# Kernel tuning notes

Hardware: AMD Instinct MI355X
Metric: run time of the kernel (lower is better)

The kernel has to match this reference:

```python
import jax, jax.numpy as jnp
import numpy as np

DIM = 768
NUM_HEADS = 12
POLY_DEG = 3
GRID = (24, 24)
BATCH = 16


def _make_powers():
    H, W = GRID
    ii, jj = np.meshgrid(np.arange(H), np.arange(W), indexing='ij')
    coords = np.stack([ii.ravel(), jj.ravel()], axis=-1).astype(np.float32)  # [HW, 2]
    dists = np.abs(coords[:, None, :] - coords[None, :, :]).sum(-1)  # L1 cdist [HW, HW]
    powers = np.stack([dists ** i for i in range(POLY_DEG + 1)], axis=0)  # [deg+1, HW, HW]
    return jnp.asarray(powers, dtype=jnp.float32)


def setup_inputs() -> dict:
    key = jax.random.key(0)
    ks = jax.random.split(key, 5)
    N = GRID[0] * GRID[1] + 1  # 577
    x = jax.random.normal(ks[0], (BATCH, N, DIM), dtype=jnp.float32)
    # nn.Linear weights stored as [in, out] for direct matmul; qkv_bias=False
    W_qkv = jax.random.normal(ks[1], (DIM, 3 * DIM), dtype=jnp.float32) * (DIM ** -0.5)
    W_proj = jax.random.normal(ks[2], (DIM, DIM), dtype=jnp.float32) * (DIM ** -0.5)
    b_proj = jnp.zeros((DIM,), dtype=jnp.float32)
    # small scale keeps polynomial bias (distances up to 46, cubed) numerically sane
    poly_coeffs = jax.random.normal(ks[3], (NUM_HEADS, POLY_DEG + 1), dtype=jnp.float32) * 0.01
    powers = _make_powers()
    return {"x": x, "W_qkv": W_qkv, "W_proj": W_proj, "b_proj": b_proj,
            "poly_coeffs": poly_coeffs, "powers": powers}


def reference(x, W_qkv, W_proj, b_proj, poly_coeffs, powers):
    B, N, C = x.shape
    h = NUM_HEADS
    d = C // h
    scale = d ** -0.5
    qkv = (x @ W_qkv).reshape(B, N, 3, h, d)
    qkv = jnp.transpose(qkv, (2, 0, 3, 1, 4))  # [3, B, h, N, d]
    q, k, v = qkv[0], qkv[1], qkv[2]
    # polynomial relative-position bias, padded with zeros for CLS row/col
    rpe = jnp.einsum('hd,dxy->hxy', poly_coeffs, powers)  # [h, HW, HW]
    rpe = jnp.pad(rpe, ((0, 0), (1, 0), (1, 0)))  # [h, N, N]
    attn = scale * jnp.einsum('bhnd,bhmd->bhnm', q, k) + rpe[None]
    attn = jax.nn.softmax(attn, axis=-1)
    out = jnp.einsum('bhnm,bhmd->bhnd', attn, v)
    out = jnp.transpose(out, (0, 2, 1, 3)).reshape(B, N, C)
    return out @ W_proj + b_proj
```

## Files before the change

kernel.cpp:

```cpp
#include <hip/hip_runtime.h>


using u16 = unsigned short;
using u32 = unsigned int;

typedef __bf16 bf16x8 __attribute__((ext_vector_type(8)));
typedef float f32x4 __attribute__((ext_vector_type(4)));

__device__ inline u16 f2bf(float f) {
    u32 u = __builtin_bit_cast(u32, f);
    u32 r = u + 0x7fffu + ((u >> 16) & 1u);
    return (u16)(r >> 16);
}
__device__ inline float bf2f(u16 x) {
    return __builtin_bit_cast(float, (u32)x << 16);
}

__device__ inline f32x4 mfma16(bf16x8 a, bf16x8 b, f32x4 c) {
    return __builtin_amdgcn_mfma_f32_16x16x32_bf16(a, b, c, 0, 0, 0);
}

__device__ inline float fexp2(float x) { return __builtin_amdgcn_exp2f(x); }

__device__ inline int xcd_remap(int bid, int nwg) {
    const int q = nwg >> 3, r = nwg & 7;
    const int xcd = bid & 7, idx = bid >> 3;
    return (xcd < r ? xcd * (q + 1) : r * (q + 1) + (xcd - r) * q) + idx;
}

__device__ inline float dpp_max16(float v) {
    int x;
    x = __builtin_amdgcn_update_dpp(0, __builtin_bit_cast(int, v), 0xB1, 0xF, 0xF, true);
    v = fmaxf(v, __builtin_bit_cast(float, x));
    x = __builtin_amdgcn_update_dpp(0, __builtin_bit_cast(int, v), 0x4E, 0xF, 0xF, true);
    v = fmaxf(v, __builtin_bit_cast(float, x));
    x = __builtin_amdgcn_update_dpp(0, __builtin_bit_cast(int, v), 0x124, 0xF, 0xF, true);
    v = fmaxf(v, __builtin_bit_cast(float, x));
    x = __builtin_amdgcn_update_dpp(0, __builtin_bit_cast(int, v), 0x128, 0xF, 0xF, true);
    v = fmaxf(v, __builtin_bit_cast(float, x));
    return v;
}
__device__ inline float dpp_sum16(float v) {
    int x;
    x = __builtin_amdgcn_update_dpp(0, __builtin_bit_cast(int, v), 0xB1, 0xF, 0xF, true);
    v += __builtin_bit_cast(float, x);
    x = __builtin_amdgcn_update_dpp(0, __builtin_bit_cast(int, v), 0x4E, 0xF, 0xF, true);
    v += __builtin_bit_cast(float, x);
    x = __builtin_amdgcn_update_dpp(0, __builtin_bit_cast(int, v), 0x124, 0xF, 0xF, true);
    v += __builtin_bit_cast(float, x);
    x = __builtin_amdgcn_update_dpp(0, __builtin_bit_cast(int, v), 0x128, 0xF, 0xF, true);
    v += __builtin_bit_cast(float, x);
    return v;
}

#define GLOAD_LDS16(g, l)                                                          \
    __builtin_amdgcn_global_load_lds((const __attribute__((address_space(1))) u32*)(g), \
                                     (__attribute__((address_space(3))) u32*)(l), 16, 0, 0)

#define BAR()    asm volatile("s_barrier" ::: "memory")
#define WAITV8() asm volatile("s_waitcnt vmcnt(8)" ::: "memory")
#define WAITV4() asm volatile("s_waitcnt vmcnt(4)" ::: "memory")
#define WAITV0() asm volatile("s_waitcnt vmcnt(0)" ::: "memory")

__global__ void k_prep(const float* __restrict__ x, const float* __restrict__ Wq,
                       const float* __restrict__ Wp, u16* __restrict__ xb,
                       u16* __restrict__ wqkv, u16* __restrict__ wprj) {
    const int tid0 = blockIdx.x * blockDim.x + threadIdx.x;
    const int stride = gridDim.x * blockDim.x;
    const int n4 = 9232 * 768 / 4;
    for (int i = tid0; i < n4; i += stride) {
        float4 v = ((const float4*)x)[i];
        ushort4 o;
        o.x = f2bf(v.x); o.y = f2bf(v.y); o.z = f2bf(v.z); o.w = f2bf(v.w);
        ((ushort4*)xb)[i] = o;
    }
    for (int i = tid0; i < 768 * 2304; i += stride) {
        int r = i / 2304, c = i - r * 2304;
        wqkv[(size_t)c * 768 + r] = f2bf(Wq[i]);
    }
    for (int i = tid0; i < 768 * 768; i += stride) {
        int r = i / 768, c = i - r * 768;
        wprj[(size_t)c * 768 + r] = f2bf(Wp[i]);
    }
}

__device__ inline void stageAB(const u16* __restrict__ Ag, const u16* __restrict__ Bg,
                               u16* L, int t) {
#pragma unroll
    for (int c = 0; c < 2; ++c) {
        const int p = c * 256 + t;
        const int row = p >> 2, ch = p & 3;
        const int src = row * 768 + ((ch ^ ((row >> 1) & 3)) * 8);
        GLOAD_LDS16(Ag + src, L + p * 8);
        GLOAD_LDS16(Bg + src, L + 4096 + p * 8);
    }
}
__device__ inline bf16x8 ldfrag32(const u16* base, int row, int slot) {
    return *(const bf16x8*)(base + row * 32 + ((slot ^ ((row >> 1) & 3)) * 8));
}

template <int MODE, int NB>
__launch_bounds__(256, 2)
__global__ void k_gemm(const u16* __restrict__ A, const u16* __restrict__ Bw,
                       u16* __restrict__ q_out, u16* __restrict__ k_out,
                       u16* __restrict__ v_out,
                       float* __restrict__ f_out, const float* __restrict__ bias) {
    constexpr int NT = 24;
    constexpr int M = 9232;
    const int wgid = xcd_remap(blockIdx.x, gridDim.x);
    const int mbase = (wgid / NB) * 128;
    const int nbase = (wgid - (wgid / NB) * NB) * 128;
    __shared__ alignas(16) u16 lds[4][8192];
    const int t = threadIdx.x;
    const int lane = t & 63, w = t >> 6;
    const int lr = lane & 15, lg = lane >> 4;
    const int wrow = (w >> 1) * 64, wcol = (w & 1) * 64;
    const u16* Ag = A + (size_t)mbase * 768;
    const u16* Bg = Bw + (size_t)nbase * 768;
    f32x4 acc[4][4] = {};

    stageAB(Ag, Bg, &lds[0][0], t);
    stageAB(Ag + 32, Bg + 32, &lds[1][0], t);
    stageAB(Ag + 64, Bg + 64, &lds[2][0], t);
    WAITV8();
    BAR();

    for (int kt = 0; kt < NT; ++kt) {
        const u16* Lc = &lds[kt & 3][0];
        if (kt + 3 < NT)
            stageAB(Ag + (kt + 3) * 32, Bg + (kt + 3) * 32, &lds[(kt + 3) & 3][0], t);
        bf16x8 af[4], bv[4];
#pragma unroll
        for (int i = 0; i < 4; ++i)
            af[i] = ldfrag32(Lc, wrow + i * 16 + lr, lg);
#pragma unroll
        for (int j = 0; j < 4; ++j)
            bv[j] = ldfrag32(Lc + 4096, wcol + j * 16 + lr, lg);
        __builtin_amdgcn_s_setprio(1);
#pragma unroll
        for (int i = 0; i < 4; ++i)
#pragma unroll
            for (int j = 0; j < 4; ++j)
                acc[i][j] = mfma16(af[i], bv[j], acc[i][j]);
        __builtin_amdgcn_s_setprio(0);
        if (kt + 1 < NT) {
            if (kt < NT - 3)       { WAITV8(); }
            else if (kt == NT - 3) { WAITV4(); }
            else                   { WAITV0(); }
            BAR();
        }
    }

#pragma unroll
    for (int i = 0; i < 4; ++i) {
#pragma unroll
        for (int j = 0; j < 4; ++j) {
            const int col = nbase + wcol + j * 16 + lr;
#pragma unroll
            for (int r = 0; r < 4; ++r) {
                const int row = mbase + wrow + i * 16 + 4 * lg + r;
                if (row < M) {
                    if (MODE == 0) {
                        const int bb = row / 577;
                        const int nn = row - bb * 577;
                        const int tt = col / 768;
                        const int rem = col - tt * 768;
                        const int hh = rem >> 6, dd = rem & 63;
                        const size_t bh = (size_t)bb * 12 + hh;
                        const u16 val = f2bf(acc[i][j][r]);
                        if (tt == 0)      q_out[(bh * 640 + nn) * 64 + dd] = val;
                        else if (tt == 1) k_out[(bh * 640 + nn) * 64 + dd] = val;
                        else              v_out[(bh * 64 + dd) * 640 + nn] = val;
                    } else {
                        f_out[(size_t)row * 768 + col] = acc[i][j][r] + bias[col];
                    }
                }
            }
        }
    }
}

__launch_bounds__(256, 3)
__global__ void k_attn(const u16* __restrict__ Qg, const u16* __restrict__ Kg,
                       const u16* __restrict__ Vtg, const float* __restrict__ coef,
                       u16* __restrict__ Og) {
    const int qt = blockIdx.x;
    const int bh = blockIdx.y;
    const int b = bh / 12, h = bh - b * 12;
    const int t = threadIdx.x;
    const int lane = t & 63, w = t >> 6;
    const int lr = lane & 15, lg = lane >> 4;
    __shared__ alignas(16) u16 Kl[2][4096];
    __shared__ alignas(16) u16 Vl[2][4096];
    __shared__ alignas(16) u16 Plds[4][16 * 72];
    __shared__ float lut[256];

    {
        const float l2e = 1.4426950408889634f;
        const float c0 = coef[h * 4 + 0] * l2e, c1 = coef[h * 4 + 1] * l2e,
                    c2 = coef[h * 4 + 2] * l2e, c3 = coef[h * 4 + 3] * l2e;
        const float d = (float)t;
        lut[t] = (t <= 46) ? (((c3 * d + c2) * d + c1) * d + c0) : 0.f;
    }

    const int qrow0 = qt * 64 + w * 16;
    const u16* qp = Qg + ((size_t)bh * 640 + qrow0 + lr) * 64;
    const bf16x8 qa0 = *(const bf16x8*)(qp + lg * 8);
    const bf16x8 qa1 = *(const bf16x8*)(qp + 32 + lg * 8);

    float gi[4], gj[4];
#pragma unroll
    for (int r = 0; r < 4; ++r) {
        const int n = qrow0 + 4 * lg + r;
        if (n == 0) { gi[r] = 100.f; gj[r] = 0.f; }
        else {
            const int nm1 = n - 1;
            const int qi = nm1 / 24;
            gi[r] = (float)qi;
            gj[r] = (float)(nm1 - qi * 24);
        }
    }

    float M[4], L[4];
#pragma unroll
    for (int r = 0; r < 4; ++r) { M[r] = -3e38f; L[r] = 0.f; }
    f32x4 acco[4] = {};
    const float scale2 = 0.125f * 1.4426950408889634f;
    const int ch0 = ((lg ^ (lr & 7))) * 8;

    const u16* Ksb = Kg + (size_t)bh * 640 * 64;
    const u16* Vsb = Vtg + (size_t)bh * 64 * 640;
    const int pr0 = t >> 3, pc0 = t & 7;
    const int pr1 = (256 + t) >> 3, pc1 = (256 + t) & 7;
    const int kd0 = pr0 * 64 + ((pc0 ^ (pr0 & 7)) * 8);
    const int kd1 = pr1 * 64 + ((pc1 ^ (pr1 & 7)) * 8);

    {
        uint4 k0 = *(const uint4*)(Ksb + pr0 * 64 + pc0 * 8);
        uint4 k1 = *(const uint4*)(Ksb + pr1 * 64 + pc1 * 8);
        uint4 v0 = *(const uint4*)(Vsb + (size_t)pr0 * 640 + pc0 * 8);
        uint4 v1 = *(const uint4*)(Vsb + (size_t)pr1 * 640 + pc1 * 8);
        *(uint4*)(&Kl[0][kd0]) = k0;
        *(uint4*)(&Kl[0][kd1]) = k1;
        *(uint4*)(&Vl[0][kd0]) = v0;
        *(uint4*)(&Vl[0][kd1]) = v1;
    }
    __syncthreads();
    int cur = 0;

    for (int kt = 0; kt < 9; ++kt) {
        const u16* Ks = Ksb + (size_t)(kt + 1) * 64 * 64;
        const u16* Vs = Vsb + (size_t)(kt + 1) * 64;
        const uint4 nk0 = *(const uint4*)(Ks + pr0 * 64 + pc0 * 8);
        const uint4 nk1 = *(const uint4*)(Ks + pr1 * 64 + pc1 * 8);
        const uint4 nv0 = *(const uint4*)(Vs + (size_t)pr0 * 640 + pc0 * 8);
        const uint4 nv1 = *(const uint4*)(Vs + (size_t)pr1 * 640 + pc1 * 8);

        const u16* Kc = &Kl[cur][0];
        const u16* Vc = &Vl[cur][0];

        f32x4 sac[4];
#pragma unroll
        for (int cb = 0; cb < 4; ++cb) {
            const int row = cb * 16 + lr;
            const bf16x8 kb0 = *(const bf16x8*)(Kc + row * 64 + ch0);
            const bf16x8 kb1 = *(const bf16x8*)(Kc + row * 64 + (ch0 ^ 32));
            f32x4 z = {};
            z = mfma16(qa0, kb0, z);
            sac[cb] = mfma16(qa1, kb1, z);
        }

        float s[4][4], tm[4];
#pragma unroll
        for (int r = 0; r < 4; ++r) tm[r] = -3e38f;
#pragma unroll
        for (int cb = 0; cb < 4; ++cb) {
            const int m = kt * 64 + cb * 16 + lr;
            float ci, cj;
            if (m == 0) { ci = 200.f; cj = 0.f; }
            else {
                const int mm1 = m - 1;
                const int pi = mm1 / 24;
                ci = (float)pi;
                cj = (float)(mm1 - pi * 24);
            }
#pragma unroll
            for (int r = 0; r < 4; ++r) {
                const float df = fabsf(gi[r] - ci) + fabsf(gj[r] - cj);
                const int idx = (int)df;
                const float v = fmaf(sac[cb][r], scale2, lut[idx]);
                s[cb][r] = v;
                tm[r] = fmaxf(tm[r], v);
            }
        }
#pragma unroll
        for (int r = 0; r < 4; ++r) tm[r] = dpp_max16(tm[r]);

        float over = tm[0] - M[0];
        over = fmaxf(over, tm[1] - M[1]);
        over = fmaxf(over, tm[2] - M[2]);
        over = fmaxf(over, tm[3] - M[3]);
        if (__any(over > 11.5f)) {
#pragma unroll
            for (int r = 0; r < 4; ++r) {
                const float Mn = fmaxf(M[r], tm[r]);
                const float a = fexp2(M[r] - Mn);
                L[r] *= a;
                acco[0][r] *= a; acco[1][r] *= a;
                acco[2][r] *= a; acco[3][r] *= a;
                M[r] = Mn;
            }
        }

        u16* pw = &Plds[w][0];
#pragma unroll
        for (int cb = 0; cb < 4; ++cb)
#pragma unroll
            for (int r = 0; r < 4; ++r) {
                const float p = fexp2(s[cb][r] - M[r]);
                L[r] += p;
                pw[(4 * lg + r) * 72 + cb * 16 + lr] = f2bf(p);
            }
        const bf16x8 pa0 = *(const bf16x8*)(pw + lr * 72 + lg * 8);
        const bf16x8 pa1 = *(const bf16x8*)(pw + lr * 72 + 32 + lg * 8);
#pragma unroll
        for (int f = 0; f < 4; ++f) {
            const int vrow = f * 16 + lr;
            const bf16x8 vb0 = *(const bf16x8*)(Vc + vrow * 64 + ch0);
            const bf16x8 vb1 = *(const bf16x8*)(Vc + vrow * 64 + (ch0 ^ 32));
            acco[f] = mfma16(pa0, vb0, acco[f]);
            acco[f] = mfma16(pa1, vb1, acco[f]);
        }

        *(uint4*)(&Kl[cur ^ 1][kd0]) = nk0;
        *(uint4*)(&Kl[cur ^ 1][kd1]) = nk1;
        *(uint4*)(&Vl[cur ^ 1][kd0]) = nv0;
        *(uint4*)(&Vl[cur ^ 1][kd1]) = nv1;
        __syncthreads();
        cur ^= 1;
    }

    {
        const u16* Kc = &Kl[cur][0];
        const u16* Vc = &Vl[cur][0];
        const bf16x8 kb0 = *(const bf16x8*)(Kc + lr * 64 + ch0);
        const bf16x8 kb1 = *(const bf16x8*)(Kc + lr * 64 + (ch0 ^ 32));
        f32x4 z = {};
        z = mfma16(qa0, kb0, z);
        const f32x4 sac0 = mfma16(qa1, kb1, z);

        float s0[4], tm[4];
#pragma unroll
        for (int r = 0; r < 4; ++r) {
            const float df = fabsf(gi[r] - 23.f) + fabsf(gj[r] - 23.f);
            float v = fmaf(sac0[r], scale2, lut[(int)df]);
            v = (lr == 0) ? v : -1e30f;
            s0[r] = v;
            tm[r] = dpp_max16(v);
        }
        float over = tm[0] - M[0];
        over = fmaxf(over, tm[1] - M[1]);
        over = fmaxf(over, tm[2] - M[2]);
        over = fmaxf(over, tm[3] - M[3]);
        if (__any(over > 11.5f)) {
#pragma unroll
            for (int r = 0; r < 4; ++r) {
                const float Mn = fmaxf(M[r], tm[r]);
                const float a = fexp2(M[r] - Mn);
                L[r] *= a;
                acco[0][r] *= a; acco[1][r] *= a;
                acco[2][r] *= a; acco[3][r] *= a;
                M[r] = Mn;
            }
        }
        u16* pw = &Plds[w][0];
#pragma unroll
        for (int cb = 0; cb < 4; ++cb)
#pragma unroll
            for (int r = 0; r < 4; ++r) {
                const float p = (cb == 0) ? fexp2(s0[r] - M[r]) : 0.f;
                L[r] += p;
                pw[(4 * lg + r) * 72 + cb * 16 + lr] = f2bf(p);
            }
        const bf16x8 pa0 = *(const bf16x8*)(pw + lr * 72 + lg * 8);
#pragma unroll
        for (int f = 0; f < 4; ++f) {
            const int vrow = f * 16 + lr;
            const bf16x8 vb0 = *(const bf16x8*)(Vc + vrow * 64 + ch0);
            acco[f] = mfma16(pa0, vb0, acco[f]);
        }
    }

    float inv[4];
#pragma unroll
    for (int r = 0; r < 4; ++r) inv[r] = __builtin_amdgcn_rcpf(dpp_sum16(L[r]));
#pragma unroll
    for (int f = 0; f < 4; ++f)
#pragma unroll
        for (int r = 0; r < 4; ++r) {
            const int n = qrow0 + 4 * lg + r;
            Og[((size_t)b * 577 + n) * 768 + h * 64 + f * 16 + lr] =
                f2bf(acco[f][r] * inv[r]);
        }
}

__launch_bounds__(256)
__global__ void k_attn_last(const u16* __restrict__ Qg, const u16* __restrict__ Kg,
                            const u16* __restrict__ Vtg, const float* __restrict__ coef,
                            u16* __restrict__ Og) {
    const int bh = blockIdx.x;
    const int b = bh / 12, h = bh - b * 12;
    const int t = threadIdx.x;
    const int lane = t & 63, w = t >> 6;
    __shared__ float qs[64];
    __shared__ float ps[640];
    __shared__ float red[4];
    __shared__ float opart[4][64];
    const float l2e = 1.4426950408889634f;
    const float c0 = coef[h * 4 + 0] * l2e, c1 = coef[h * 4 + 1] * l2e,
                c2 = coef[h * 4 + 2] * l2e, c3 = coef[h * 4 + 3] * l2e;
    const float scale2 = 0.125f * l2e;

    if (t < 64) qs[t] = bf2f(Qg[((size_t)bh * 640 + 576) * 64 + t]);
    __syncthreads();

    float sv[3];
#pragma unroll
    for (int u = 0; u < 3; ++u) {
        const int k = t + u * 256;
        float s = -3e38f;
        if (k < 577) {
            const u16* kp = Kg + ((size_t)bh * 640 + k) * 64;
            float acc = 0.f;
            for (int j = 0; j < 64; ++j) acc += qs[j] * bf2f(kp[j]);
            float rv = 0.f;
            if (k >= 1) {
                const int km1 = k - 1;
                const int ki = km1 / 24;
                const float d = fabsf(23.f - (float)ki) + fabsf(23.f - (float)(km1 - ki * 24));
                rv = ((c3 * d + c2) * d + c1) * d + c0;
            }
            s = fmaf(acc, scale2, rv);
        }
        sv[u] = s;
    }
    float v = fmaxf(fmaxf(sv[0], sv[1]), sv[2]);
    v = fmaxf(v, __shfl_xor(v, 1));  v = fmaxf(v, __shfl_xor(v, 2));
    v = fmaxf(v, __shfl_xor(v, 4));  v = fmaxf(v, __shfl_xor(v, 8));
    v = fmaxf(v, __shfl_xor(v, 16)); v = fmaxf(v, __shfl_xor(v, 32));
    if (lane == 0) red[w] = v;
    __syncthreads();
    const float Mx = fmaxf(fmaxf(red[0], red[1]), fmaxf(red[2], red[3]));

    float lsum = 0.f;
#pragma unroll
    for (int u = 0; u < 3; ++u) {
        const int k = t + u * 256;
        const float p = (k < 577) ? fexp2(sv[u] - Mx) : 0.f;
        if (k < 640) ps[k] = p;
        lsum += p;
    }
    lsum += __shfl_xor(lsum, 1);  lsum += __shfl_xor(lsum, 2);
    lsum += __shfl_xor(lsum, 4);  lsum += __shfl_xor(lsum, 8);
    lsum += __shfl_xor(lsum, 16); lsum += __shfl_xor(lsum, 32);
    __syncthreads();
    if (lane == 0) red[w] = lsum;
    __syncthreads();
    const float Lx = red[0] + red[1] + red[2] + red[3];

    const int d = t & 63, qd = t >> 6;
    const u16* vp = Vtg + ((size_t)bh * 64 + d) * 640;
    float o = 0.f;
    for (int k = qd * 160; k < qd * 160 + 160; ++k) o += ps[k] * bf2f(vp[k]);
    opart[qd][d] = o;
    __syncthreads();
    if (t < 64) {
        const float oo = (opart[0][t] + opart[1][t] + opart[2][t] + opart[3][t]) / Lx;
        Og[((size_t)b * 577 + 576) * 768 + h * 64 + t] = f2bf(oo);
    }
}

extern "C" void kernel_launch(void* const* d_in, const int* in_sizes, int n_in,
                              void* d_out, int out_size, void* d_ws, size_t ws_size,
                              hipStream_t stream) {
    const float* x      = (const float*)d_in[0];
    const float* W_qkv  = (const float*)d_in[1];
    const float* W_proj = (const float*)d_in[2];
    const float* b_proj = (const float*)d_in[3];
    const float* coef   = (const float*)d_in[4];
    float* out = (float*)d_out;
    char* ws = (char*)d_ws;

    u16* xb   = (u16*)(ws + 0);
    u16* Og   = (u16*)(ws + 0);
    u16* wqkv = (u16*)(ws + 14180352);
    u16* wprj = (u16*)(ws + 17719296);
    u16* Qg   = (u16*)(ws + 18898944);
    u16* Kg   = (u16*)(ws + 34627584);
    u16* Vtg  = (u16*)(ws + 50356224);

    k_prep<<<2048, 256, 0, stream>>>(x, W_qkv, W_proj, xb, wqkv, wprj);

    k_gemm<0, 18><<<18 * 73, 256, 0, stream>>>(xb, wqkv, Qg, Kg, Vtg,
                                               nullptr, nullptr);
    k_attn<<<dim3(9, 192), 256, 0, stream>>>(Qg, Kg, Vtg, coef, Og);
    k_attn_last<<<192, 256, 0, stream>>>(Qg, Kg, Vtg, coef, Og);
    k_gemm<1, 6><<<6 * 73, 256, 0, stream>>>(Og, wprj, nullptr, nullptr,
                                             nullptr, out, b_proj);
}
```

Baseline: 183.7 us.

## Tile weight transpose in prep, remap attention grid, reuse V buffer for P

```diff
diff --git a/kernel.cpp b/kernel.cpp
--- a/kernel.cpp
+++ b/kernel.cpp
@@ -65,22 +65,46 @@
 __global__ void k_prep(const float* __restrict__ x, const float* __restrict__ Wq,
                        const float* __restrict__ Wp, u16* __restrict__ xb,
                        u16* __restrict__ wqkv, u16* __restrict__ wprj) {
-    const int tid0 = blockIdx.x * blockDim.x + threadIdx.x;
-    const int stride = gridDim.x * blockDim.x;
-    const int n4 = 9232 * 768 / 4;
-    for (int i = tid0; i < n4; i += stride) {
-        float4 v = ((const float4*)x)[i];
-        ushort4 o;
-        o.x = f2bf(v.x); o.y = f2bf(v.y); o.z = f2bf(v.z); o.w = f2bf(v.w);
-        ((ushort4*)xb)[i] = o;
-    }
-    for (int i = tid0; i < 768 * 2304; i += stride) {
-        int r = i / 2304, c = i - r * 2304;
-        wqkv[(size_t)c * 768 + r] = f2bf(Wq[i]);
-    }
-    for (int i = tid0; i < 768 * 768; i += stride) {
-        int r = i / 768, c = i - r * 768;
-        wprj[(size_t)c * 768 + r] = f2bf(Wp[i]);
+    const int bid = blockIdx.x;
+    const int t = threadIdx.x;
+    if (bid < 576) {
+        __shared__ float tile[64][65];
+        const float* src;
+        u16* dst;
+        int C, rt, ct;
+        if (bid < 432) { src = Wq; dst = wqkv; C = 2304; rt = bid / 36; ct = bid % 36; }
+        else { const int b2 = bid - 432; src = Wp; dst = wprj; C = 768; rt = b2 / 12; ct = b2 % 12; }
+        const int row0 = rt * 64, col0 = ct * 64;
+#pragma unroll
+        for (int it = 0; it < 4; ++it) {
+            const int row = it * 16 + (t >> 4);
+            const float4 v = *(const float4*)&src[(size_t)(row0 + row) * C + col0 + (t & 15) * 4];
+            tile[row][(t & 15) * 4 + 0] = v.x;
+            tile[row][(t & 15) * 4 + 1] = v.y;
+            tile[row][(t & 15) * 4 + 2] = v.z;
+            tile[row][(t & 15) * 4 + 3] = v.w;
+        }
+        __syncthreads();
+#pragma unroll
+        for (int it = 0; it < 4; ++it) {
+            const int oc = it * 16 + (t >> 4);
+            const int orr = (t & 15) * 4;
+            ushort4 o;
+            o.x = f2bf(tile[orr + 0][oc]);
+            o.y = f2bf(tile[orr + 1][oc]);
+            o.z = f2bf(tile[orr + 2][oc]);
+            o.w = f2bf(tile[orr + 3][oc]);
+            *(ushort4*)&dst[(size_t)(col0 + oc) * 768 + row0 + orr] = o;
+        }
+    } else {
+        const int n4 = 9232 * 768 / 4;
+        const int stride = (2048 - 576) * 256;
+        for (int i = (bid - 576) * 256 + t; i < n4; i += stride) {
+            float4 v = ((const float4*)x)[i];
+            ushort4 o;
+            o.x = f2bf(v.x); o.y = f2bf(v.y); o.z = f2bf(v.z); o.w = f2bf(v.w);
+            ((ushort4*)xb)[i] = o;
+        }
     }
 }
 
@@ -180,27 +204,29 @@
     }
 }
 
-__launch_bounds__(256, 3)
+__launch_bounds__(256, 4)
 __global__ void k_attn(const u16* __restrict__ Qg, const u16* __restrict__ Kg,
                        const u16* __restrict__ Vtg, const float* __restrict__ coef,
                        u16* __restrict__ Og) {
-    const int qt = blockIdx.x;
-    const int bh = blockIdx.y;
+    const int wgid = xcd_remap(blockIdx.x, gridDim.x);
+    const int bh = wgid / 9;
+    const int qt = wgid - bh * 9;
     const int b = bh / 12, h = bh - b * 12;
     const int t = threadIdx.x;
     const int lane = t & 63, w = t >> 6;
     const int lr = lane & 15, lg = lane >> 4;
     __shared__ alignas(16) u16 Kl[2][4096];
     __shared__ alignas(16) u16 Vl[2][4096];
-    __shared__ alignas(16) u16 Plds[4][16 * 72];
-    __shared__ float lut[256];
+    __shared__ float lut[48];
 
     {
         const float l2e = 1.4426950408889634f;
         const float c0 = coef[h * 4 + 0] * l2e, c1 = coef[h * 4 + 1] * l2e,
                     c2 = coef[h * 4 + 2] * l2e, c3 = coef[h * 4 + 3] * l2e;
-        const float d = (float)t;
-        lut[t] = (t <= 46) ? (((c3 * d + c2) * d + c1) * d + c0) : 0.f;
+        if (t < 48) {
+            const float d = (float)t;
+            lut[t] = (t <= 46) ? (((c3 * d + c2) * d + c1) * d + c0) : 0.f;
+        }
     }
 
     const int qrow0 = qt * 64 + w * 16;
@@ -234,16 +260,20 @@
     const int pr1 = (256 + t) >> 3, pc1 = (256 + t) & 7;
     const int kd0 = pr0 * 64 + ((pc0 ^ (pr0 & 7)) * 8);
     const int kd1 = pr1 * 64 + ((pc1 ^ (pr1 & 7)) * 8);
+    const int vr0 = 16 * w + (lane >> 3), vc = lane & 7;
+    const int vr1 = vr0 + 8;
+    const int vd0 = vr0 * 64 + ((vc ^ (vr0 & 7)) * 8);
+    const int vd1 = vr1 * 64 + ((vc ^ (vr1 & 7)) * 8);
 
     {
         uint4 k0 = *(const uint4*)(Ksb + pr0 * 64 + pc0 * 8);
         uint4 k1 = *(const uint4*)(Ksb + pr1 * 64 + pc1 * 8);
-        uint4 v0 = *(const uint4*)(Vsb + (size_t)pr0 * 640 + pc0 * 8);
-        uint4 v1 = *(const uint4*)(Vsb + (size_t)pr1 * 640 + pc1 * 8);
+        uint4 v0 = *(const uint4*)(Vsb + (size_t)vr0 * 640 + vc * 8);
+        uint4 v1 = *(const uint4*)(Vsb + (size_t)vr1 * 640 + vc * 8);
         *(uint4*)(&Kl[0][kd0]) = k0;
         *(uint4*)(&Kl[0][kd1]) = k1;
-        *(uint4*)(&Vl[0][kd0]) = v0;
-        *(uint4*)(&Vl[0][kd1]) = v1;
+        *(uint4*)(&Vl[0][vd0]) = v0;
+        *(uint4*)(&Vl[0][vd1]) = v1;
     }
     __syncthreads();
     int cur = 0;
@@ -253,13 +283,15 @@
         const u16* Vs = Vsb + (size_t)(kt + 1) * 64;
         const uint4 nk0 = *(const uint4*)(Ks + pr0 * 64 + pc0 * 8);
         const uint4 nk1 = *(const uint4*)(Ks + pr1 * 64 + pc1 * 8);
-        const uint4 nv0 = *(const uint4*)(Vs + (size_t)pr0 * 640 + pc0 * 8);
-        const uint4 nv1 = *(const uint4*)(Vs + (size_t)pr1 * 640 + pc1 * 8);
+        const uint4 nv0 = *(const uint4*)(Vs + (size_t)vr0 * 640 + vc * 8);
+        const uint4 nv1 = *(const uint4*)(Vs + (size_t)vr1 * 640 + vc * 8);
 
         const u16* Kc = &Kl[cur][0];
         const u16* Vc = &Vl[cur][0];
+        u16* pw = &Vl[cur ^ 1][w * 1024];
 
         f32x4 sac[4];
+        __builtin_amdgcn_s_setprio(1);
 #pragma unroll
         for (int cb = 0; cb < 4; ++cb) {
             const int row = cb * 16 + lr;
@@ -269,6 +301,7 @@
             z = mfma16(qa0, kb0, z);
             sac[cb] = mfma16(qa1, kb1, z);
         }
+        __builtin_amdgcn_s_setprio(0);
 
         float s[4][4], tm[4];
 #pragma unroll
@@ -287,7 +320,7 @@
 #pragma unroll
             for (int r = 0; r < 4; ++r) {
                 const float df = fabsf(gi[r] - ci) + fabsf(gj[r] - cj);
-                const int idx = (int)df;
+                const int idx = min((int)df, 47);
                 const float v = fmaf(sac[cb][r], scale2, lut[idx]);
                 s[cb][r] = v;
                 tm[r] = fmaxf(tm[r], v);
@@ -312,17 +345,18 @@
             }
         }
 
-        u16* pw = &Plds[w][0];
 #pragma unroll
         for (int cb = 0; cb < 4; ++cb)
 #pragma unroll
             for (int r = 0; r < 4; ++r) {
                 const float p = fexp2(s[cb][r] - M[r]);
                 L[r] += p;
-                pw[(4 * lg + r) * 72 + cb * 16 + lr] = f2bf(p);
-            }
-        const bf16x8 pa0 = *(const bf16x8*)(pw + lr * 72 + lg * 8);
-        const bf16x8 pa1 = *(const bf16x8*)(pw + lr * 72 + 32 + lg * 8);
+                const int rw = 4 * lg + r;
+                pw[rw * 64 + (((2 * cb + (lr >> 3)) ^ (rw & 7)) * 8) + (lr & 7)] = f2bf(p);
+            }
+        const bf16x8 pa0 = *(const bf16x8*)(pw + lr * 64 + ch0);
+        const bf16x8 pa1 = *(const bf16x8*)(pw + lr * 64 + (ch0 ^ 32));
+        __builtin_amdgcn_s_setprio(1);
 #pragma unroll
         for (int f = 0; f < 4; ++f) {
             const int vrow = f * 16 + lr;
@@ -331,11 +365,12 @@
             acco[f] = mfma16(pa0, vb0, acco[f]);
             acco[f] = mfma16(pa1, vb1, acco[f]);
         }
+        __builtin_amdgcn_s_setprio(0);
 
         *(uint4*)(&Kl[cur ^ 1][kd0]) = nk0;
         *(uint4*)(&Kl[cur ^ 1][kd1]) = nk1;
-        *(uint4*)(&Vl[cur ^ 1][kd0]) = nv0;
-        *(uint4*)(&Vl[cur ^ 1][kd1]) = nv1;
+        *(uint4*)(&Vl[cur ^ 1][vd0]) = nv0;
+        *(uint4*)(&Vl[cur ^ 1][vd1]) = nv1;
         __syncthreads();
         cur ^= 1;
     }
@@ -343,6 +378,7 @@
     {
         const u16* Kc = &Kl[cur][0];
         const u16* Vc = &Vl[cur][0];
+        u16* pw = &Vl[cur ^ 1][w * 1024];
         const bf16x8 kb0 = *(const bf16x8*)(Kc + lr * 64 + ch0);
         const bf16x8 kb1 = *(const bf16x8*)(Kc + lr * 64 + (ch0 ^ 32));
         f32x4 z = {};
@@ -353,7 +389,7 @@
 #pragma unroll
         for (int r = 0; r < 4; ++r) {
             const float df = fabsf(gi[r] - 23.f) + fabsf(gj[r] - 23.f);
-            float v = fmaf(sac0[r], scale2, lut[(int)df]);
+            float v = fmaf(sac0[r], scale2, lut[min((int)df, 47)]);
             v = (lr == 0) ? v : -1e30f;
             s0[r] = v;
             tm[r] = dpp_max16(v);
@@ -373,16 +409,16 @@
                 M[r] = Mn;
             }
         }
-        u16* pw = &Plds[w][0];
 #pragma unroll
         for (int cb = 0; cb < 4; ++cb)
 #pragma unroll
             for (int r = 0; r < 4; ++r) {
                 const float p = (cb == 0) ? fexp2(s0[r] - M[r]) : 0.f;
                 L[r] += p;
-                pw[(4 * lg + r) * 72 + cb * 16 + lr] = f2bf(p);
-            }
-        const bf16x8 pa0 = *(const bf16x8*)(pw + lr * 72 + lg * 8);
+                const int rw = 4 * lg + r;
+                pw[rw * 64 + (((2 * cb + (lr >> 3)) ^ (rw & 7)) * 8) + (lr & 7)] = f2bf(p);
+            }
+        const bf16x8 pa0 = *(const bf16x8*)(pw + lr * 64 + ch0);
 #pragma unroll
         for (int f = 0; f < 4; ++f) {
             const int vrow = f * 16 + lr;
@@ -503,7 +539,7 @@
 
     k_gemm<0, 18><<<18 * 73, 256, 0, stream>>>(xb, wqkv, Qg, Kg, Vtg,
                                                nullptr, nullptr);
-    k_attn<<<dim3(9, 192), 256, 0, stream>>>(Qg, Kg, Vtg, coef, Og);
+    k_attn<<<1728, 256, 0, stream>>>(Qg, Kg, Vtg, coef, Og);
     k_attn_last<<<192, 256, 0, stream>>>(Qg, Kg, Vtg, coef, Og);
     k_gemm<1, 6><<<6 * 73, 256, 0, stream>>>(Og, wprj, nullptr, nullptr,
                                              nullptr, out, b_proj);
```

Result: faster. 171.9 us (-6.4%).
